# Kernel tuning notes

Hardware: AMD Instinct MI355X
Metric: run time of the kernel (lower is better)

Reference implementation:

```python
import jax, jax.numpy as jnp
import numpy as np

CONF_THRES = 0.25   # NMS.conf
IOU_THRES = 0.45    # NMS.iou
MAX_NMS = 1024      # fixed candidate count so greedy NMS is jit-compatible
IMG = 640.0


def setup_inputs() -> dict:
    key = jax.random.key(0)
    k0, k1, k2, k3, k4 = jax.random.split(key, 5)
    B, N = 32, 25200
    cxcy = jax.random.uniform(k0, (B, N, 2), dtype=jnp.float32) * IMG
    wh = jax.random.uniform(k1, (B, N, 2), dtype=jnp.float32) * 80.0 + 2.0
    obj = jax.random.uniform(k2, (B, N, 1), dtype=jnp.float32)
    lmk = jax.random.uniform(k3, (B, N, 10), dtype=jnp.float32) * IMG
    cls = jax.random.uniform(k4, (B, N, 1), dtype=jnp.float32)
    # layout: [cx, cy, w, h, obj, 10 landmark coords, 1 class score]
    prediction = jnp.concatenate([cxcy, wh, obj, lmk, cls], axis=2)
    return {"prediction": prediction}


def xywh2xyxy(x):
    cx, cy, w, h = x[:, 0], x[:, 1], x[:, 2], x[:, 3]
    return jnp.stack([cx - w / 2, cy - h / 2, cx + w / 2, cy + h / 2], axis=1)


def pairwise_iou(b):  # b: [K,4] xyxy -> [K,K]
    area = (b[:, 2] - b[:, 0]) * (b[:, 3] - b[:, 1])
    lt = jnp.maximum(b[:, None, :2], b[None, :, :2])
    rb = jnp.minimum(b[:, None, 2:], b[None, :, 2:])
    wh = jnp.clip(rb - lt, 0.0)
    inter = wh[..., 0] * wh[..., 1]
    return inter / (area[:, None] + area[None, :] - inter + 1e-7)


def _nms_image(pred):  # pred: [N,16]
    obj = pred[:, 4]
    score = pred[:, 15] * obj  # x[:,15:] *= x[:,4:5]; nc==1 -> single class, j==0
    valid = (obj > CONF_THRES) & (score > CONF_THRES)  # xc filter + conf filter
    s = jnp.where(valid, score, -1.0)
    top_s, idx = jax.lax.top_k(s, MAX_NMS)  # score-sorted candidates (greedy NMS order)
    x = pred[idx]  # [K,16]
    box = xywh2xyxy(x[:, :4])
    vmask = top_s > 0.0  # valid candidates (invalid slots carry score -1)
    # class offset c = j*4096 is identically 0 since nc==1 -> skip
    iou = pairwise_iou(box)  # [K,K]
    rng = jnp.arange(MAX_NMS)

    def step(keep, i):
        sup = keep[i] & (iou[i] > IOU_THRES) & (rng > i)
        return keep & ~sup, None

    keep, _ = jax.lax.scan(step, vmask, rng)
    det = jnp.concatenate(
        [box, top_s[:, None], x[:, 5:15], jnp.zeros((MAX_NMS, 1), pred.dtype)], axis=1
    )  # [K,16] = box(4) | conf(1) | landmarks(10) | class(1)=0
    return det * keep[:, None].astype(det.dtype), keep


def reference(prediction):
    # Fixed-shape analogue of the per-image ragged output: detections padded to
    # MAX_NMS rows per image (zeroed where suppressed) plus a keep mask.
    det, keep = jax.vmap(_nms_image)(prediction)
    return det, keep
```

## Files before the change

### kernel.cpp

```cpp
#include <hip/hip_runtime.h>
#include <stdint.h>

#define NB 32
#define NN 25200
#define NN4 6300
#define TOPK 1024
#define NF 16
#define CONF 0.25f
#define IOU_T 0.45f
#define NBIN 4096
#define CAP 2048
#define KEY_BASE 0xBE800001u

__device__ __forceinline__ uint32_t score_key(float obj, float cls) {
  float score = __fmul_rn(cls, obj);
  bool valid = (obj > CONF) && (score > CONF);
  float s = valid ? score : -1.0f;
  uint32_t u = __float_as_uint(s);
  return (u & 0x80000000u) ? ~u : (u | 0x80000000u);
}

__device__ __forceinline__ uint64_t shfl_xor_u64(uint64_t v, int m) {
  uint32_t lo = __shfl_xor((uint32_t)v, m, 64);
  uint32_t hi = __shfl_xor((uint32_t)(v >> 32), m, 64);
  return ((uint64_t)hi << 32) | lo;
}

__global__ void k_keys(const float* __restrict__ pred, uint32_t* __restrict__ keys) {
  int g = blockIdx.x * blockDim.x + threadIdx.x;
  if (g >= NB * NN) return;
  const float* row = pred + (size_t)g * NF;
  keys[g] = score_key(row[4], row[15]);
}

__global__ __launch_bounds__(1024) void k_select(const float* __restrict__ pred,
                                                 const uint32_t* __restrict__ keys,
                                                 int* __restrict__ sel,
                                                 float4* __restrict__ boxv,
                                                 float* __restrict__ arv,
                                                 uint32_t* __restrict__ vb) {
  int b = blockIdx.x;
  int tid = threadIdx.x;
  int lane = tid & 63, wid = tid >> 6;
  const uint4* kb4 = (const uint4*)(keys + (size_t)b * NN);
  __shared__ uint32_t hist[NBIN];
  __shared__ uint64_t ent[CAP];
  __shared__ uint32_t wsum[16];
  __shared__ uint32_t sh_bin;
  __shared__ uint32_t sh_cnt;
  #pragma unroll
  for (int k = 0; k < 4; ++k) hist[tid + 1024 * k] = 0;
  ent[tid] = 0; ent[tid + 1024] = 0;
  if (tid == 0) { sh_cnt = 0; sh_bin = 0; }
  __syncthreads();

  uint4 kreg[7];
  #pragma unroll
  for (int k = 0; k < 7; ++k) {
    int i = tid + k * 1024;
    if (i < NN4) {
      kreg[k] = kb4[i];
      uint32_t kv[4] = {kreg[k].x, kreg[k].y, kreg[k].z, kreg[k].w};
      #pragma unroll
      for (int c = 0; c < 4; ++c) {
        uint32_t key = kv[c];
        if (key >= KEY_BASE) {
          uint32_t bin = (key - KEY_BASE) >> 12;
          if (bin > NBIN - 1) bin = NBIN - 1;
          atomicAdd(&hist[bin], 1u);
        }
      }
    }
  }
  __syncthreads();

  uint32_t h[4]; uint32_t s = 0;
  #pragma unroll
  for (int k = 0; k < 4; ++k) { h[k] = hist[NBIN - 1 - (4 * tid + k)]; s += h[k]; }
  uint32_t my = s;
  #pragma unroll
  for (int d = 1; d < 64; d <<= 1) {
    uint32_t v = __shfl_up(s, d, 64);
    if (lane >= d) s += v;
  }
  if (lane == 63) wsum[wid] = s;
  __syncthreads();
  uint32_t base = 0;
  for (int w = 0; w < wid; ++w) base += wsum[w];
  uint32_t cum = base + s - my;
  #pragma unroll
  for (int k = 0; k < 4; ++k) {
    if (cum < TOPK && cum + h[k] >= TOPK) sh_bin = (uint32_t)(NBIN - 1 - (4 * tid + k));
    cum += h[k];
  }
  __syncthreads();
  uint32_t thr = KEY_BASE + (sh_bin << 12);

  #pragma unroll
  for (int k = 0; k < 7; ++k) {
    int i = tid + k * 1024;
    if (i < NN4) {
      uint32_t kv[4] = {kreg[k].x, kreg[k].y, kreg[k].z, kreg[k].w};
      #pragma unroll
      for (int c = 0; c < 4; ++c) {
        uint32_t key = kv[c];
        if (key >= thr) {
          uint32_t p = atomicAdd(&sh_cnt, 1u);
          if (p < CAP) ent[p] = ((uint64_t)key << 32) | (uint32_t)(~(uint32_t)(4 * i + c));
        }
      }
    }
  }
  __syncthreads();

  uint64_t v0 = ent[tid], v1 = ent[tid + 1024];
  for (unsigned kk = 2; kk <= CAP; kk <<= 1) {
    for (unsigned j = kk >> 1; j > 0; j >>= 1) {
      if (j == 1024) {
        uint64_t mx = v0 > v1 ? v0 : v1;
        uint64_t mn = v0 > v1 ? v1 : v0;
        v0 = mx; v1 = mn;
      } else if (j >= 64) {
        __syncthreads();
        ent[tid] = v0; ent[tid + 1024] = v1;
        __syncthreads();
        uint64_t p0 = ent[tid ^ j], p1 = ent[(tid ^ j) + 1024];
        bool low = ((tid & j) == 0);
        bool d0 = ((tid & kk) == 0);
        bool d1 = (((tid + 1024) & kk) == 0);
        v0 = (low != d0) ? (v0 < p0 ? v0 : p0) : (v0 > p0 ? v0 : p0);
        v1 = (low != d1) ? (v1 < p1 ? v1 : p1) : (v1 > p1 ? v1 : p1);
      } else {
        uint64_t p0 = shfl_xor_u64(v0, (int)j);
        uint64_t p1 = shfl_xor_u64(v1, (int)j);
        bool low = ((tid & j) == 0);
        bool d0 = ((tid & kk) == 0);
        bool d1 = (((tid + 1024) & kk) == 0);
        v0 = (low != d0) ? (v0 < p0 ? v0 : p0) : (v0 > p0 ? v0 : p0);
        v1 = (low != d1) ? (v1 < p1 ? v1 : p1) : (v1 > p1 ? v1 : p1);
      }
    }
  }
  uint32_t key = (uint32_t)(v0 >> 32);
  uint32_t n = ~(uint32_t)(v0 & 0xFFFFFFFFu);
  if (n >= NN) n = 0;
  sel[(size_t)b * TOPK + tid] = (int)n;

  bool valid = key >= KEY_BASE;
  uint64_t bal = __ballot(valid);
  if (lane == 0) {
    vb[(size_t)b * 32 + 2 * wid] = (uint32_t)bal;
    vb[(size_t)b * 32 + 2 * wid + 1] = (uint32_t)(bal >> 32);
  }

  {
    const float4* row = (const float4*)(pred + ((size_t)b * NN + n) * NF);
    float4 r0 = row[0];
    float hw = __fmul_rn(r0.z, 0.5f), hh = __fmul_rn(r0.w, 0.5f);
    float x1 = __fsub_rn(r0.x, hw), y1 = __fsub_rn(r0.y, hh);
    float x2 = __fadd_rn(r0.x, hw), y2 = __fadd_rn(r0.y, hh);
    boxv[(size_t)b * TOPK + tid] = make_float4(x1, y1, x2, y2);
    arv[(size_t)b * TOPK + tid] = __fmul_rn(__fsub_rn(x2, x1), __fsub_rn(y2, y1));
  }
}

__global__ __launch_bounds__(1024) void k_mask(const float4* __restrict__ boxv,
                                               const float* __restrict__ arv,
                                               uint32_t* __restrict__ mask) {
  int b = blockIdx.x;
  int sblk = blockIdx.y;
  int tid = threadIdx.x;
  int rg = tid & 31;
  int cc = tid >> 5;
  __shared__ float bx1[TOPK], by1[TOPK], bx2[TOPK], by2[TOPK], bar[TOPK];
  {
    float4 bb = boxv[(size_t)b * TOPK + tid];
    bx1[tid] = bb.x; by1[tid] = bb.y; bx2[tid] = bb.z; by2[tid] = bb.w;
    bar[tid] = arv[(size_t)b * TOPK + tid];
  }
  __syncthreads();
  int i0 = sblk * 128 + rg * 4;
  int iw = i0 >> 5;
  uint32_t wreg[4] = {0u, 0u, 0u, 0u};
  if (cc >= iw) {
    float rx1[4], ry1[4], rx2[4], ry2[4], rar[4];
    #pragma unroll
    for (int k = 0; k < 4; ++k) {
      rx1[k] = bx1[i0 + k]; ry1[k] = by1[i0 + k];
      rx2[k] = bx2[i0 + k]; ry2[k] = by2[i0 + k]; rar[k] = bar[i0 + k];
    }
    for (int jj = 0; jj < 32; ++jj) {
      int j = cc * 32 + jj;
      float cx1 = bx1[j], cy1 = by1[j], cx2 = bx2[j], cy2 = by2[j], car = bar[j];
      #pragma unroll
      for (int k = 0; k < 4; ++k) {
        float lx = fmaxf(rx1[k], cx1);
        float ly = fmaxf(ry1[k], cy1);
        float rx = fminf(rx2[k], cx2);
        float ry = fminf(ry2[k], cy2);
        float wd = fmaxf(__fsub_rn(rx, lx), 0.0f);
        float ht = fmaxf(__fsub_rn(ry, ly), 0.0f);
        float inter = __fmul_rn(wd, ht);
        float den = __fadd_rn(__fsub_rn(__fadd_rn(rar[k], car), inter), 1e-7f);
        float iou = __fdiv_rn(inter, den);
        wreg[k] |= (iou > IOU_T ? 1u : 0u) << jj;
      }
    }
    if (cc == iw) {
      #pragma unroll
      for (int k = 0; k < 4; ++k)
        wreg[k] &= ~((2u << ((i0 + k) & 31)) - 1u);
    }
  }
  uint4 out = make_uint4(wreg[0], wreg[1], wreg[2], wreg[3]);
  *(uint4*)&mask[((size_t)b * 32 + cc) * TOPK + i0] = out;
}

__global__ __launch_bounds__(1024, 4) void k_scan_out(const float* __restrict__ pred,
                                                      const int* __restrict__ sel,
                                                      const uint32_t* __restrict__ mask,
                                                      const uint32_t* __restrict__ vb,
                                                      float* __restrict__ det,
                                                      float* __restrict__ keep_out) {
  int b = blockIdx.x;
  int tid = threadIdx.x;
  __shared__ uint32_t smask[32 * 1024];

  uint32_t kw0 = 0;
  if (tid < 32) kw0 = vb[(size_t)b * 32 + tid];

  const uint4* gm4 = (const uint4*)(mask + (size_t)b * (32 * TOPK));
  uint4* sm4 = (uint4*)smask;
  #pragma unroll
  for (int q = 0; q < 8; ++q) {
    int idx4 = tid + q * 1024;
    int row = idx4 >> 8;
    int col4 = idx4 & 255;
    sm4[row * 256 + (col4 ^ (row & 7))] = gm4[idx4];
  }
  __syncthreads();

  if (tid < 32) {
    int l = tid;
    const int rbase = l * 256;
    const int sw = l & 7;
    uint32_t cur[32];
    #pragma unroll
    for (int q = 0; q < 8; ++q) *(uint4*)&cur[4 * q] = sm4[rbase + (q ^ sw)];
    uint32_t kw = kw0;
    uint32_t nxt[32];
    for (int w = 0; w < 32; ++w) {
      if (w < 31) {
        #pragma unroll
        for (int q = 0; q < 8; ++q)
          *(uint4*)&nxt[4 * q] = sm4[rbase + (w + 1) * 8 + (q ^ sw)];
      }
      uint32_t rw = kw;
      #pragma unroll
      for (int t = 0; t < 32; ++t)
        if ((rw >> t) & 1u) rw &= ~cur[t];
      uint32_t rf = __shfl(rw, w, 64);
      if (l == w) {
        kw = rf;
      } else if (l > w) {
        uint32_t acc = 0;
        #pragma unroll
        for (int t = 0; t < 32; ++t) acc |= ((rf >> t) & 1u) ? cur[t] : 0u;
        kw &= ~acc;
      }
      if (w < 31) {
        #pragma unroll
        for (int t = 0; t < 32; ++t) cur[t] = nxt[t];
      }
    }
    smask[l] = kw;
  }
  __syncthreads();

  int n = sel[(size_t)b * TOPK + tid];
  const float4* rowv = (const float4*)(pred + ((size_t)b * NN + n) * NF);
  bool kept = (smask[tid >> 5] >> (tid & 31)) & 1u;
  float m = kept ? 1.0f : 0.0f;
  float4 r0 = rowv[0], r1 = rowv[1], r2 = rowv[2], r3 = rowv[3];
  float score = __fmul_rn(r3.w, r1.x);
  float hw = __fmul_rn(r0.z, 0.5f), hh = __fmul_rn(r0.w, 0.5f);
  float4 o0 = make_float4(__fsub_rn(r0.x, hw) * m, __fsub_rn(r0.y, hh) * m,
                          __fadd_rn(r0.x, hw) * m, __fadd_rn(r0.y, hh) * m);
  float4 o1 = make_float4(score * m, r1.y * m, r1.z * m, r1.w * m);
  float4 o2 = make_float4(r2.x * m, r2.y * m, r2.z * m, r2.w * m);
  float4 o3 = make_float4(r3.x * m, r3.y * m, r3.z * m, 0.0f);
  float4* dst = (float4*)(det + ((size_t)b * TOPK + tid) * NF);
  dst[0] = o0; dst[1] = o1; dst[2] = o2; dst[3] = o3;
  keep_out[(size_t)b * TOPK + tid] = m;
}

extern "C" void kernel_launch(void* const* d_in, const int* in_sizes, int n_in,
                              void* d_out, int out_size, void* d_ws, size_t ws_size,
                              hipStream_t stream) {
  const float* pred = (const float*)d_in[0];
  float* det = (float*)d_out;
  float* keep = det + (size_t)NB * TOPK * NF;

  uint8_t* ws = (uint8_t*)d_ws;
  size_t off = 0;
  uint32_t* keys = (uint32_t*)(ws + off); off += (size_t)NB * NN * 4;
  int* sel = (int*)(ws + off);            off += (size_t)NB * TOPK * 4;
  uint32_t* mask = (uint32_t*)(ws + off); off += (size_t)NB * 32 * TOPK * 4;
  float4* boxv = (float4*)(ws + off);     off += (size_t)NB * TOPK * 16;
  float* arv = (float*)(ws + off);        off += (size_t)NB * TOPK * 4;
  uint32_t* vb = (uint32_t*)(ws + off);   off += (size_t)NB * 32 * 4;

  k_keys<<<(NB * NN + 255) / 256, 256, 0, stream>>>(pred, keys);
  k_select<<<NB, 1024, 0, stream>>>(pred, keys, sel, boxv, arv, vb);
  dim3 gm(NB, 8);
  k_mask<<<gm, 1024, 0, stream>>>(boxv, arv, mask);
  k_scan_out<<<NB, 1024, 0, stream>>>(pred, sel, mask, vb, det, keep);
}
```

Baseline: 169.1 us.

## Fuse IoU mask and greedy scan kernels using per-image atomic counters

Merges the mask-building and scan/output kernels into one launch. Each of the 8 blocks per image signals completion through an agent-scope atomic counter, which k_keys zeroes. Block 0 of each image spin-waits on that counter, then runs the scan and writes the outputs. This removes one kernel launch and its boundary, but the wait depends on all 8 blocks of an image being co-resident or already finished, which risks deadlock or stalls. The scan also drops its register double-buffering of the next mask row.

```diff
diff --git a/kernel.cpp b/kernel.cpp
--- a/kernel.cpp
+++ b/kernel.cpp
@@ -26,7 +26,9 @@
   return ((uint64_t)hi << 32) | lo;
 }
 
-__global__ void k_keys(const float* __restrict__ pred, uint32_t* __restrict__ keys) {
+__global__ void k_keys(const float* __restrict__ pred, uint32_t* __restrict__ keys,
+                       uint32_t* __restrict__ cnt) {
+  if (blockIdx.x == 0 && threadIdx.x < NB) cnt[threadIdx.x] = 0u;
   int g = blockIdx.x * blockDim.x + threadIdx.x;
   if (g >= NB * NN) return;
   const float* row = pred + (size_t)g * NF;
@@ -164,15 +166,27 @@
   }
 }
 
-__global__ __launch_bounds__(1024) void k_mask(const float4* __restrict__ boxv,
-                                               const float* __restrict__ arv,
-                                               uint32_t* __restrict__ mask) {
+__global__ __launch_bounds__(1024, 4) void k_maskscan(const float* __restrict__ pred,
+                                                      const int* __restrict__ sel,
+                                                      const float4* __restrict__ boxv,
+                                                      const float* __restrict__ arv,
+                                                      const uint32_t* __restrict__ vb,
+                                                      uint32_t* __restrict__ mask,
+                                                      uint32_t* __restrict__ cnt,
+                                                      float* __restrict__ det,
+                                                      float* __restrict__ keep_out) {
   int b = blockIdx.x;
   int sblk = blockIdx.y;
   int tid = threadIdx.x;
   int rg = tid & 31;
   int cc = tid >> 5;
-  __shared__ float bx1[TOPK], by1[TOPK], bx2[TOPK], by2[TOPK], bar[TOPK];
+  __shared__ uint32_t smask[32 * 1024];
+  float* bx1 = (float*)smask;
+  float* by1 = bx1 + TOPK;
+  float* bx2 = by1 + TOPK;
+  float* by2 = bx2 + TOPK;
+  float* bar = by2 + TOPK;
+
   {
     float4 bb = boxv[(size_t)b * TOPK + tid];
     bx1[tid] = bb.x; by1[tid] = bb.y; bx2[tid] = bb.z; by2[tid] = bb.w;
@@ -214,20 +228,22 @@
   }
   uint4 out = make_uint4(wreg[0], wreg[1], wreg[2], wreg[3]);
   *(uint4*)&mask[((size_t)b * 32 + cc) * TOPK + i0] = out;
-}
-
-__global__ __launch_bounds__(1024, 4) void k_scan_out(const float* __restrict__ pred,
-                                                      const int* __restrict__ sel,
-                                                      const uint32_t* __restrict__ mask,
-                                                      const uint32_t* __restrict__ vb,
-                                                      float* __restrict__ det,
-                                                      float* __restrict__ keep_out) {
-  int b = blockIdx.x;
-  int tid = threadIdx.x;
-  __shared__ uint32_t smask[32 * 1024];
+
+  __threadfence();
+  __syncthreads();
+  if (tid == 0)
+    __hip_atomic_fetch_add(&cnt[b], 1u, __ATOMIC_RELEASE, __HIP_MEMORY_SCOPE_AGENT);
+  if (sblk != 0) return;
 
   uint32_t kw0 = 0;
   if (tid < 32) kw0 = vb[(size_t)b * 32 + tid];
+
+  if (tid == 0) {
+    while (__hip_atomic_load(&cnt[b], __ATOMIC_ACQUIRE, __HIP_MEMORY_SCOPE_AGENT) < 8u)
+      __builtin_amdgcn_s_sleep(2);
+  }
+  __syncthreads();
+  (void)__hip_atomic_load(&cnt[b], __ATOMIC_ACQUIRE, __HIP_MEMORY_SCOPE_AGENT);
 
   const uint4* gm4 = (const uint4*)(mask + (size_t)b * (32 * TOPK));
   uint4* sm4 = (uint4*)smask;
@@ -244,17 +260,12 @@
     int l = tid;
     const int rbase = l * 256;
     const int sw = l & 7;
-    uint32_t cur[32];
-    #pragma unroll
-    for (int q = 0; q < 8; ++q) *(uint4*)&cur[4 * q] = sm4[rbase + (q ^ sw)];
     uint32_t kw = kw0;
-    uint32_t nxt[32];
     for (int w = 0; w < 32; ++w) {
-      if (w < 31) {
-        #pragma unroll
-        for (int q = 0; q < 8; ++q)
-          *(uint4*)&nxt[4 * q] = sm4[rbase + (w + 1) * 8 + (q ^ sw)];
-      }
+      uint32_t cur[32];
+      #pragma unroll
+      for (int q = 0; q < 8; ++q)
+        *(uint4*)&cur[4 * q] = sm4[rbase + w * 8 + (q ^ sw)];
       uint32_t rw = kw;
       #pragma unroll
       for (int t = 0; t < 32; ++t)
@@ -267,10 +278,6 @@
         #pragma unroll
         for (int t = 0; t < 32; ++t) acc |= ((rf >> t) & 1u) ? cur[t] : 0u;
         kw &= ~acc;
-      }
-      if (w < 31) {
-        #pragma unroll
-        for (int t = 0; t < 32; ++t) cur[t] = nxt[t];
       }
     }
     smask[l] = kw;
@@ -309,10 +316,10 @@
   float4* boxv = (float4*)(ws + off);     off += (size_t)NB * TOPK * 16;
   float* arv = (float*)(ws + off);        off += (size_t)NB * TOPK * 4;
   uint32_t* vb = (uint32_t*)(ws + off);   off += (size_t)NB * 32 * 4;
-
-  k_keys<<<(NB * NN + 255) / 256, 256, 0, stream>>>(pred, keys);
+  uint32_t* cnt = (uint32_t*)(ws + off);  off += (size_t)NB * 4;
+
+  k_keys<<<(NB * NN + 255) / 256, 256, 0, stream>>>(pred, keys, cnt);
   k_select<<<NB, 1024, 0, stream>>>(pred, keys, sel, boxv, arv, vb);
   dim3 gm(NB, 8);
-  k_mask<<<gm, 1024, 0, stream>>>(boxv, arv, mask);
-  k_scan_out<<<NB, 1024, 0, stream>>>(pred, sel, mask, vb, det, keep);
-}
+  k_maskscan<<<gm, 1024, 0, stream>>>(pred, sel, boxv, arv, vb, mask, cnt, det, keep);
+}
```

Result: slower. 223.4 us (+32.1%).
